# Optimization experiments

Hardware: AMD Instinct MI355X
Metric: run time of the kernel (lower is better)

Reference implementation:

```python
import jax, jax.numpy as jnp
import numpy as np

EPS = 1e-6

def _conv(x, w, padding):
    # x: [B,C,H,W], w: [O,I,kh,kw]
    return jax.lax.conv_general_dilated(x, w, window_strides=(1, 1), padding=padding,
                                        dimension_numbers=('NCHW', 'OIHW', 'NCHW'))

def setup_inputs() -> dict:
    key = jax.random.key(0)
    ks = jax.random.split(key, 8)
    C = 512
    B, H, W = 4, 64, 64
    s1 = 1.0 / np.sqrt(C)          # 1x1 conv fan-in
    s3 = 1.0 / np.sqrt(C * 9)      # 3x3 conv fan-in
    return {
        'x': jax.random.normal(ks[0], (B, C, H, W), dtype=jnp.float32),
        'ln_w': jnp.ones((C,), dtype=jnp.float32),
        'ln_b': jnp.zeros((C,), dtype=jnp.float32),
        'wq': jax.random.normal(ks[1], (C, C, 1, 1), dtype=jnp.float32) * s1,
        'wk': jax.random.normal(ks[2], (C, C, 3, 3), dtype=jnp.float32) * s3,
        'wv': jax.random.normal(ks[3], (C, C, 3, 3), dtype=jnp.float32) * s3,
        'wp': jax.random.normal(ks[4], (C, C, 1, 1), dtype=jnp.float32) * s1,
        'bp': jnp.zeros((C,), dtype=jnp.float32),
    }

def reference(x, ln_w, ln_b, wq, wk, wv, wp, bp):
    # channels_first LayerNorm over C
    u = jnp.mean(x, axis=1, keepdims=True)
    s = jnp.mean((x - u) ** 2, axis=1, keepdims=True)
    h = (x - u) / jnp.sqrt(s + EPS)
    h = ln_w[None, :, None, None] * h + ln_b[None, :, None, None]

    q = _conv(h, wq, 'VALID')           # 1x1
    k = _conv(h, wk, [(1, 1), (1, 1)])  # 3x3, pad 1
    v = _conv(h, wv, [(1, 1), (1, 1)])

    b, c, H, W = q.shape
    hw = H * W
    q = q.reshape(b, c, hw)
    k = k.reshape(b, c, hw)
    v = v.reshape(b, c, hw)

    scale = jnp.asarray(int(c) ** (-0.5), q.dtype)
    attn = jnp.einsum('bcm,bcn->bmn', q, k) * scale  # [b, hw_q, hw_k]
    attn = jax.nn.softmax(attn, axis=2)
    out = jnp.einsum('bcn,bmn->bcm', v, attn)        # [b, c, hw_q]
    out = out.reshape(b, c, H, W)

    out = _conv(out, wp, 'VALID') + bp[None, :, None, None]
    return x + out
```

## Files before the change

kernel.cpp:

```cpp
#include <hip/hip_runtime.h>
#include <hip/hip_bf16.h>

#define C_DIM 512
#define HW    4096
#define BATCH 4
#define PW    66
#define PPIX  (PW*PW)

typedef __attribute__((ext_vector_type(8))) short bf16x8;
typedef __attribute__((ext_vector_type(4))) float f32x4;
typedef __attribute__((ext_vector_type(16))) float f32x16;
typedef __attribute__((ext_vector_type(2))) long long l64x2;

static __device__ __forceinline__ short f2b(float f) {
    union { float f; unsigned u; } v; v.f = f;
    unsigned r = v.u + 0x7fffu + ((v.u >> 16) & 1u);
    return (short)(r >> 16);
}
static __device__ __forceinline__ float b2f(short s) {
    union { unsigned u; float f; } v; v.u = ((unsigned)(unsigned short)s) << 16;
    return v.f;
}

static __device__ __forceinline__ f32x4 zero4() {
    f32x4 v = {0.f, 0.f, 0.f, 0.f};
    return v;
}
static __device__ __forceinline__ f32x16 zero16() {
    f32x16 v = {0.f,0.f,0.f,0.f, 0.f,0.f,0.f,0.f, 0.f,0.f,0.f,0.f, 0.f,0.f,0.f,0.f};
    return v;
}

static __device__ __forceinline__ void gload16(const void* g, void* l) {
    __builtin_amdgcn_global_load_lds(
        (__attribute__((address_space(1))) void*)g,
        (__attribute__((address_space(3))) void*)l, 16, 0, 0);
}

__global__ void k_cvt_bf16(const float* __restrict__ in, short* __restrict__ out, int n) {
    int i = blockIdx.x * 256 + threadIdx.x;
    if (i < n) out[i] = f2b(in[i]);
}

__global__ void k_reorder_w38(const float* __restrict__ w, unsigned char* __restrict__ out) {
    int i = blockIdx.x * 256 + threadIdx.x;
    int o = i / 576;
    int p8 = (i - o * 576) * 8;
    int kc2 = p8 >> 6;
    int tap = kc2 >> 3;
    int p = p8 & 63;
    int g = (p >> 4) & 3, half = (p >> 3) & 1;
    int c0 = (kc2 & 7) * 64 + half * 32 + g * 8;
    const float* src = w + ((size_t)o * 512 + c0) * 9 + tap;
    float f0 = src[0] * 64.f, f1 = src[9] * 64.f, f2 = src[18] * 64.f, f3 = src[27] * 64.f;
    float f4 = src[36] * 64.f, f5 = src[45] * 64.f, f6 = src[54] * 64.f, f7 = src[63] * 64.f;
    int lo = __builtin_amdgcn_cvt_pk_fp8_f32(f0, f1, 0, false);
    lo     = __builtin_amdgcn_cvt_pk_fp8_f32(f2, f3, lo, true);
    int hi = __builtin_amdgcn_cvt_pk_fp8_f32(f4, f5, 0, false);
    hi     = __builtin_amdgcn_cvt_pk_fp8_f32(f6, f7, hi, true);
    *(uint2*)&out[(size_t)o * 4608 + p8] = make_uint2((unsigned)lo, (unsigned)hi);
}

__global__ void k_cvt_h8(const short* __restrict__ hp, unsigned char* __restrict__ out) {
    int i = blockIdx.x * 256 + threadIdx.x;
    int row = i >> 6;
    int p8 = (i & 63) * 8;
    int grp = p8 >> 6;
    int p = p8 & 63;
    int g = (p >> 4) & 3, half = (p >> 3) & 1;
    int c = grp * 64 + half * 32 + g * 8;
    bf16x8 v = *(const bf16x8*)&hp[(size_t)row * 512 + c];
    int lo = __builtin_amdgcn_cvt_pk_fp8_f32(b2f(v[0]), b2f(v[1]), 0, false);
    lo     = __builtin_amdgcn_cvt_pk_fp8_f32(b2f(v[2]), b2f(v[3]), lo, true);
    int hi = __builtin_amdgcn_cvt_pk_fp8_f32(b2f(v[4]), b2f(v[5]), 0, false);
    hi     = __builtin_amdgcn_cvt_pk_fp8_f32(b2f(v[6]), b2f(v[7]), hi, true);
    *(uint2*)&out[(size_t)row * 512 + p8] = make_uint2((unsigned)lo, (unsigned)hi);
}

__global__ void k_cvt_k8(const short* __restrict__ in, unsigned char* __restrict__ out) {
    int i = blockIdx.x * 256 + threadIdx.x;
    int m = i >> 6;
    int p = (i & 63) * 8;
    int kcp = p >> 6, g = (p >> 4) & 3, half = (p >> 3) & 1;
    int chb = (kcp * 2 + half) * 32 + g * 8;
    bf16x8 v = *(const bf16x8*)&in[(size_t)m * 512 + chb];
    int lo = __builtin_amdgcn_cvt_pk_fp8_f32(b2f(v[0]), b2f(v[1]), 0, false);
    lo     = __builtin_amdgcn_cvt_pk_fp8_f32(b2f(v[2]), b2f(v[3]), lo, true);
    int hi = __builtin_amdgcn_cvt_pk_fp8_f32(b2f(v[4]), b2f(v[5]), 0, false);
    hi     = __builtin_amdgcn_cvt_pk_fp8_f32(b2f(v[6]), b2f(v[7]), hi, true);
    *(uint2*)&out[(size_t)m * 512 + p] = make_uint2((unsigned)lo, (unsigned)hi);
}

__global__ void k_ln_fused(const float* __restrict__ x, const float* __restrict__ lnw,
                           const float* __restrict__ lnb, short* __restrict__ hp) {
    __shared__ float red[8][64];
    __shared__ float mean_s[64], rstd_s[64];
    __shared__ short tile[64][65];
    int bid = blockIdx.x;
    int y = bid & 63, b = bid >> 6;
    int t = threadIdx.x;
    int px = t & 63, cg = t >> 6;
    const float* xb = x + (size_t)b * C_DIM * HW + (size_t)y * 64;

    float s = 0.f, sq = 0.f;
    for (int c = cg * 128; c < cg * 128 + 128; ++c) {
        float v = xb[(size_t)c * HW + px];
        s += v; sq += v * v;
    }
    red[cg][px] = s;
    red[4 + cg][px] = sq;
    __syncthreads();
    if (t < 64) {
        float S = red[0][t] + red[1][t] + red[2][t] + red[3][t];
        float Q = red[4][t] + red[5][t] + red[6][t] + red[7][t];
        float mu  = S * (1.0f / C_DIM);
        float var = Q * (1.0f / C_DIM) - mu * mu;
        mean_s[t] = mu;
        rstd_s[t] = 1.0f / sqrtf(var + 1e-6f);
    }
    __syncthreads();
    float mu = mean_s[px], rs = rstd_s[px];
    int cj = t & 63, pj = t >> 6;
    for (int ct = 0; ct < 8; ++ct) {
        int c0 = ct * 64;
        #pragma unroll
        for (int cc = 0; cc < 64; cc += 4) {
            int c = c0 + cc + cg;
            float v = xb[(size_t)c * HW + px];
            tile[cc + cg][px] = f2b((v - mu) * rs * lnw[c] + lnb[c]);
        }
        __syncthreads();
        #pragma unroll
        for (int pp = 0; pp < 64; pp += 4) {
            int pidx = pp + pj;
            size_t dst = ((size_t)b * PPIX + (size_t)(y + 1) * PW + 1 + pidx) * C_DIM + c0 + cj;
            hp[dst] = tile[cj][pidx];
        }
        __syncthreads();
    }
}

template<int TAPS, int GMODE, int EPI>
__global__ __launch_bounds__(256, 2) void k_gemm(
        const short* __restrict__ A, const short* __restrict__ Bw,
        void* __restrict__ Out, const float* __restrict__ bias,
        const float* __restrict__ resid)
{
    constexpr int K = TAPS * 512;
    constexpr int NKC = K / 64;
    __shared__ short Alds[128 * 64];
    __shared__ short Blds[128 * 64];
    int bid = blockIdx.x;
    int mt = bid & 31, nt = (bid >> 5) & 3, b = bid >> 7;
    int m0 = mt * 128, n0 = nt * 128;
    int t = threadIdx.x;
    int lane = t & 63, w = t >> 6;
    int wm = w >> 1, wn = w & 1;
    int g = lane >> 4, li = lane & 15;
    int srow = t >> 3, schunk = t & 7;
    const short* Ab = A + (GMODE == 0 ? (size_t)b * PPIX * C_DIM : (size_t)b * HW * C_DIM);

    f32x4 acc[4][4];
    #pragma unroll
    for (int i = 0; i < 4; ++i)
        #pragma unroll
        for (int j = 0; j < 4; ++j) acc[i][j] = zero4();

    for (int kc = 0; kc < NKC; ++kc) {
        int tap = (TAPS == 9) ? (kc >> 3) : 4;
        int cb  = (kc & 7) * 64;
        __syncthreads();
        #pragma unroll
        for (int r = 0; r < 4; ++r) {
            int row = r * 32 + srow;
            size_t goff;
            if (GMODE == 0) {
                int m = m0 + row;
                int yy = m >> 6, xx = m & 63;
                int pp = (yy + tap / 3) * PW + xx + (tap % 3);
                goff = (size_t)pp * C_DIM + cb + schunk * 8;
            } else {
                goff = (size_t)(m0 + row) * K + kc * 64 + schunk * 8;
            }
            gload16(Ab + goff, Alds + row * 64 + schunk * 8);
        }
        #pragma unroll
        for (int r = 0; r < 4; ++r) {
            int row = r * 32 + srow;
            size_t goff = (size_t)(n0 + row) * K + kc * 64 + schunk * 8;
            gload16(Bw + goff, Blds + row * 64 + schunk * 8);
        }
        __syncthreads();
        #pragma unroll
        for (int ks = 0; ks < 2; ++ks) {
            int koff = ks * 32 + g * 8;
            bf16x8 af[4], bfr[4];
            #pragma unroll
            for (int i = 0; i < 4; ++i)
                af[i] = *(const bf16x8*)&Alds[(wm * 64 + i * 16 + li) * 64 + koff];
            #pragma unroll
            for (int j = 0; j < 4; ++j)
                bfr[j] = *(const bf16x8*)&Blds[(wn * 64 + j * 16 + li) * 64 + koff];
            #pragma unroll
            for (int i = 0; i < 4; ++i)
                #pragma unroll
                for (int j = 0; j < 4; ++j)
                    acc[i][j] = __builtin_amdgcn_mfma_f32_16x16x32_bf16(af[i], bfr[j], acc[i][j], 0, 0, 0);
        }
    }
    #pragma unroll
    for (int fm = 0; fm < 4; ++fm) {
        #pragma unroll
        for (int fn = 0; fn < 4; ++fn) {
            int mrow = m0 + wm * 64 + fm * 16 + g * 4;
            int ncol = n0 + wn * 64 + fn * 16 + li;
            if constexpr (EPI == 0) {
                #pragma unroll
                for (int i = 0; i < 4; ++i) {
                    size_t dst = ((size_t)b * HW + mrow + i) * C_DIM + ncol;
                    ((short*)Out)[dst] = f2b(acc[fm][fn][i]);
                }
            } else if constexpr (EPI == 1) {
                size_t dst = ((size_t)b * C_DIM + ncol) * HW + mrow;
                short4 sv = make_short4(f2b(acc[fm][fn][0]), f2b(acc[fm][fn][1]),
                                        f2b(acc[fm][fn][2]), f2b(acc[fm][fn][3]));
                *(short4*)((short*)Out + dst) = sv;
            } else {
                size_t dst = ((size_t)b * C_DIM + ncol) * HW + mrow;
                float bb = bias[ncol];
                float4 xr = *(const float4*)(resid + dst);
                float4 o;
                o.x = acc[fm][fn][0] + bb + xr.x;
                o.y = acc[fm][fn][1] + bb + xr.y;
                o.z = acc[fm][fn][2] + bb + xr.z;
                o.w = acc[fm][fn][3] + bb + xr.w;
                *(float4*)((float*)Out + dst) = o;
            }
        }
    }
}

__global__ __launch_bounds__(256, 2) void k_gemm_kv8(
        const unsigned char* __restrict__ A8, const unsigned char* __restrict__ Bk8,
        const unsigned char* __restrict__ Bv8, short* __restrict__ OutK,
        short* __restrict__ OutV)
{
    __shared__ unsigned char Alds[2][10240];
    __shared__ unsigned char Bklds[2][10240];
    __shared__ unsigned char Bvlds[2][10240];
    int bid = blockIdx.x;
    int mt = bid & 31, nt = (bid >> 5) & 3, b = bid >> 7;
    int m0 = mt * 128, n0 = nt * 128;
    int t = threadIdx.x;
    int lane = t & 63, w = t >> 6;
    int wm = w >> 1, wn = w & 1;
    int g = lane >> 4, li = lane & 15;
    const unsigned char* Ab = A8 + (size_t)b * PPIX * 512;

    int srowv[3], schv[3];
    #pragma unroll
    for (int r = 0; r < 3; ++r) {
        int slot = r * 256 + t;
        int row = slot / 5;
        int ch = slot - row * 5;
        srowv[r] = row;
        schv[r] = (ch < 4) ? ch * 16 : 0;
    }
    bool act2 = (w < 2);

    f32x4 accK[4][4], accV[4][4];
    #pragma unroll
    for (int i = 0; i < 4; ++i)
        #pragma unroll
        for (int j = 0; j < 4; ++j) { accK[i][j] = zero4(); accV[i][j] = zero4(); }

    auto STAGE = [&](int bf, int kc2) {
        int tap = kc2 >> 3;
        int gofs = (kc2 & 7) * 64;
        int ty3 = tap / 3, tx3 = tap % 3;
        #pragma unroll
        for (int r = 0; r < 3; ++r) {
            if (r < 2 || act2) {
                int row = srowv[r];
                int m = m0 + row;
                int yy = m >> 6, xx = m & 63;
                int pp = (yy + ty3) * PW + xx + tx3;
                int dst = (r * 256 + t) * 16;
                gload16(Ab + (size_t)pp * 512 + gofs + schv[r], &Alds[bf][dst]);
                size_t gb = (size_t)(n0 + row) * 4608 + kc2 * 64 + schv[r];
                gload16(Bk8 + gb, &Bklds[bf][dst]);
                gload16(Bv8 + gb, &Bvlds[bf][dst]);
            }
        }
    };

    auto COMPUTE = [&](int bf) {
        l64x2 av[4], bk[4], bv[4];
        #pragma unroll
        for (int i = 0; i < 4; ++i)
            av[i] = *(const l64x2*)&Alds[bf][(wm * 64 + i * 16 + li) * 80 + g * 16];
        #pragma unroll
        for (int j = 0; j < 4; ++j)
            bk[j] = *(const l64x2*)&Bklds[bf][(wn * 64 + j * 16 + li) * 80 + g * 16];
        #pragma unroll
        for (int j = 0; j < 4; ++j)
            bv[j] = *(const l64x2*)&Bvlds[bf][(wn * 64 + j * 16 + li) * 80 + g * 16];
        #pragma unroll
        for (int h = 0; h < 2; ++h) {
            #pragma unroll
            for (int i = 0; i < 4; ++i)
                #pragma unroll
                for (int j = 0; j < 4; ++j)
                    accK[i][j] = __builtin_amdgcn_mfma_f32_16x16x32_fp8_fp8(
                        av[i][h], bk[j][h], accK[i][j], 0, 0, 0);
            #pragma unroll
            for (int i = 0; i < 4; ++i)
                #pragma unroll
                for (int j = 0; j < 4; ++j)
                    accV[i][j] = __builtin_amdgcn_mfma_f32_16x16x32_fp8_fp8(
                        av[i][h], bv[j][h], accV[i][j], 0, 0, 0);
        }
    };

    STAGE(0, 0);
    __syncthreads();
    int bf = 0;
    for (int kc2 = 0; kc2 < 72; ++kc2) {
        if (kc2 + 1 < 72) STAGE(bf ^ 1, kc2 + 1);
        COMPUTE(bf);
        __syncthreads();
        bf ^= 1;
    }

    const float SCL = 0.015625f;
    #pragma unroll
    for (int fm = 0; fm < 4; ++fm) {
        #pragma unroll
        for (int fn = 0; fn < 4; ++fn) {
            int mrow = m0 + wm * 64 + fm * 16 + g * 4;
            int ncol = n0 + wn * 64 + fn * 16 + li;
            #pragma unroll
            for (int i = 0; i < 4; ++i) {
                size_t dst = ((size_t)b * HW + mrow + i) * C_DIM + ncol;
                OutK[dst] = f2b(accK[fm][fn][i] * SCL);
            }
            size_t dstv = ((size_t)b * C_DIM + ncol) * HW + mrow;
            short4 sv = make_short4(f2b(accV[fm][fn][0] * SCL), f2b(accV[fm][fn][1] * SCL),
                                    f2b(accV[fm][fn][2] * SCL), f2b(accV[fm][fn][3] * SCL));
            *(short4*)(OutV + dstv) = sv;
        }
    }
}

#define KT 32
#define NTILES 64
__global__ __launch_bounds__(512, 2) void k_attn(
        const short* __restrict__ qT, const unsigned char* __restrict__ kT8,
        const short* __restrict__ vg, short* __restrict__ O0,
        short* __restrict__ O1, float* __restrict__ L0, float* __restrict__ L1)
{
    __shared__ __align__(16) short pool[73728];
    unsigned char* Kp8 = (unsigned char*)pool;
    short* Vp = pool + 16384;
    short* Pp = pool + 57344;

    int bid0 = blockIdx.x;
    int bid = (bid0 & 7) * 32 + (bid0 >> 3);
    int qt = bid & 31, ks = (bid >> 5) & 1, b = bid >> 6;
    int m0 = qt * 128;
    int t = threadIdx.x, lane = t & 63, w = t >> 6;
    int g = lane >> 4, li = lane & 15;
    int l31 = lane & 31, l5 = lane >> 5;

    const unsigned char* kb8 = kT8 + ((size_t)b * HW + (size_t)ks * 2048) * 512;
    const short* vb = vg + (size_t)b * C_DIM * HW + ks * 2048;

    long long qf8[16];
    {
        const short* qrow = qT + ((size_t)b * HW + m0 + w * 16 + li) * C_DIM;
        #pragma unroll
        for (int kc = 0; kc < 16; ++kc) {
            bf16x8 qv = *(const bf16x8*)&qrow[kc * 32 + g * 8];
            int lo = __builtin_amdgcn_cvt_pk_fp8_f32(b2f(qv[0]), b2f(qv[1]), 0, false);
            lo     = __builtin_amdgcn_cvt_pk_fp8_f32(b2f(qv[2]), b2f(qv[3]), lo, true);
            int hi = __builtin_amdgcn_cvt_pk_fp8_f32(b2f(qv[4]), b2f(qv[5]), 0, false);
            hi     = __builtin_amdgcn_cvt_pk_fp8_f32(b2f(qv[6]), b2f(qv[7]), hi, true);
            qf8[kc] = ((long long)(unsigned)hi << 32) | (unsigned)lo;
        }
    }
    f32x16 oacc[8];
    #pragma unroll
    for (int a = 0; a < 8; ++a) oacc[a] = zero16();
    float lsum = 0.f;

    const unsigned char* ksrc8 = kb8 + (size_t)(t & 31) * 512 + (t >> 5) * 16;
    int voff[5];
    #pragma unroll
    for (int r = 0; r < 5; ++r) {
        int D = r * 512 + t;
        int ch = D / 5;
        int c  = D - ch * 5;
        voff[r] = (c < 4) ? ch * 4096 + c * 8 : 0;
    }

    const float SC = 0.044194173824159216f * 1.4426950408889634f;

    auto STAGE = [&](int buf, int nt) {
        int n0 = nt * KT;
        const unsigned char* kS = ksrc8 + (size_t)n0 * 512;
        unsigned char* kD = Kp8 + buf * 16384 + t * 16;
        gload16(kS, kD);
        gload16(kS + 256, kD + 8192);
        short* vD = Vp + buf * 20480 + t * 8;
        #pragma unroll
        for (int r = 0; r < 5; ++r)
            gload16(vb + voff[r] + n0, vD + r * 4096);
    };

    STAGE(0, 0);
    asm volatile("s_waitcnt vmcnt(0)" ::: "memory");
    __builtin_amdgcn_s_barrier();
    __builtin_amdgcn_sched_barrier(0);

    int buf = 0;
    for (int nt = 0; nt < NTILES; ++nt) {
        if (nt + 1 < NTILES) STAGE(buf ^ 1, nt + 1);

        const unsigned char* kbase8 = Kp8 + buf * 16384 + g * 512 + li * 16;
        f32x4 s0[2], s1[2];
        s0[0] = zero4(); s0[1] = zero4(); s1[0] = zero4(); s1[1] = zero4();
        __builtin_amdgcn_s_setprio(1);
        #pragma unroll
        for (int kcp = 0; kcp < 8; ++kcp) {
            #pragma unroll
            for (int fn = 0; fn < 2; ++fn) {
                l64x2 kv = *(const l64x2*)&kbase8[kcp * 2048 + fn * 256];
                s0[fn] = __builtin_amdgcn_mfma_f32_16x16x32_fp8_fp8(kv[0], qf8[2 * kcp],     s0[fn], 0, 0, 0);
                s1[fn] = __builtin_amdgcn_mfma_f32_16x16x32_fp8_fp8(kv[1], qf8[2 * kcp + 1], s1[fn], 0, 0, 0);
            }
        }
        __builtin_amdgcn_s_setprio(0);
        #pragma unroll
        for (int fn = 0; fn < 2; ++fn) {
            float e0 = exp2f((s0[fn][0] + s1[fn][0]) * SC);
            float e1 = exp2f((s0[fn][1] + s1[fn][1]) * SC);
            float e2 = exp2f((s0[fn][2] + s1[fn][2]) * SC);
            float e3 = exp2f((s0[fn][3] + s1[fn][3]) * SC);
            lsum += (e0 + e1) + (e2 + e3);
            union { __hip_bfloat162 h; unsigned u; } p01, p23;
            p01.h = __float22bfloat162_rn(make_float2(e0, e1));
            p23.h = __float22bfloat162_rn(make_float2(e2, e3));
            *(uint2*)&Pp[(w * 16 + li) * 40 + fn * 16 + g * 4] = make_uint2(p01.u, p23.u);
        }

        asm volatile("s_waitcnt lgkmcnt(0)" ::: "memory");
        __builtin_amdgcn_s_barrier();
        __builtin_amdgcn_sched_barrier(0);

        const short* vbase = Vp + buf * 20480 + (size_t)w * 64 * 40;
        bf16x8 vf[2][2];
        #pragma unroll
        for (int cht = 0; cht < 2; ++cht)
            #pragma unroll
            for (int kx = 0; kx < 2; ++kx)
                vf[cht][kx] = *(const bf16x8*)&vbase[(cht * 32 + l31) * 40 + kx * 16 + l5 * 8];
        __builtin_amdgcn_s_setprio(1);
        #pragma unroll
        for (int q2 = 0; q2 < 4; ++q2) {
            #pragma unroll
            for (int kx = 0; kx < 2; ++kx) {
                bf16x8 pf = *(const bf16x8*)&Pp[(q2 * 32 + l31) * 40 + kx * 16 + l5 * 8];
                oacc[q2 * 2 + 0] = __builtin_amdgcn_mfma_f32_32x32x16_bf16(vf[0][kx], pf, oacc[q2 * 2 + 0], 0, 0, 0);
                oacc[q2 * 2 + 1] = __builtin_amdgcn_mfma_f32_32x32x16_bf16(vf[1][kx], pf, oacc[q2 * 2 + 1], 0, 0, 0);
            }
        }
        __builtin_amdgcn_s_setprio(0);

        asm volatile("s_waitcnt vmcnt(0)" ::: "memory");
        __builtin_amdgcn_s_barrier();
        __builtin_amdgcn_sched_barrier(0);
        buf ^= 1;
    }

    lsum += __shfl_xor(lsum, 16);
    lsum += __shfl_xor(lsum, 32);
    float* Lb = (ks ? L1 : L0) + (size_t)b * HW + m0 + w * 16;
    if (lane < 16) Lb[lane] = lsum;

    short* tp = pool + w * 9216;
    #pragma unroll
    for (int a = 0; a < 8; ++a) {
        int q2 = a >> 1, cht = a & 1;
        int q_l = q2 * 32 + l31;
        #pragma unroll
        for (int rq = 0; rq < 4; ++rq) {
            int chb = cht * 32 + rq * 8 + l5 * 4;
            union { __hip_bfloat162 h; unsigned u; } x01, x23;
            x01.h = __float22bfloat162_rn(make_float2(oacc[a][rq * 4 + 0], oacc[a][rq * 4 + 1]));
            x23.h = __float22bfloat162_rn(make_float2(oacc[a][rq * 4 + 2], oacc[a][rq * 4 + 3]));
            *(uint2*)&tp[q_l * 72 + chb] = make_uint2(x01.u, x23.u);
        }
    }
    asm volatile("s_waitcnt lgkmcnt(0)" ::: "memory");
    __builtin_amdgcn_sched_barrier(0);
    short* Ob = (ks ? O1 : O0) + ((size_t)b * HW + m0) * C_DIM + w * 64;
    #pragma unroll
    for (int qg = 0; qg < 16; ++qg) {
        int qr = qg * 8 + (lane >> 3);
        bf16x8 v = *(const bf16x8*)&tp[qr * 72 + (lane & 7) * 8];
        *(bf16x8*)&Ob[(size_t)qr * C_DIM + (lane & 7) * 8] = v;
    }
}

__global__ void k_att_comb(const short* __restrict__ O0, const short* __restrict__ O1,
                           const float* __restrict__ L0, const float* __restrict__ L1,
                           short* __restrict__ oatt) {
    int i = blockIdx.x * 256 + threadIdx.x;
    int row = i >> 6;
    int c0 = (i & 63) * 8;
    float r = 1.0f / (L0[row] + L1[row]);
    size_t base = (size_t)row * C_DIM + c0;
    bf16x8 a = *(const bf16x8*)&O0[base];
    bf16x8 c = *(const bf16x8*)&O1[base];
    bf16x8 o;
    #pragma unroll
    for (int j = 0; j < 8; ++j)
        o[j] = f2b((b2f(a[j]) + b2f(c[j])) * r);
    *(bf16x8*)&oatt[base] = o;
}

extern "C" void kernel_launch(void* const* d_in, const int* in_sizes, int n_in,
                              void* d_out, int out_size, void* d_ws, size_t ws_size,
                              hipStream_t stream) {
    const float* x    = (const float*)d_in[0];
    const float* ln_w = (const float*)d_in[1];
    const float* ln_b = (const float*)d_in[2];
    const float* wq   = (const float*)d_in[3];
    const float* wk   = (const float*)d_in[4];
    const float* wv   = (const float*)d_in[5];
    const float* wp   = (const float*)d_in[6];
    const float* bp   = (const float*)d_in[7];
    float* out = (float*)d_out;

    char* ws = (char*)d_ws;
    size_t off = 0;
    auto alloc = [&](size_t bytes) {
        char* p = ws + off;
        off += (bytes + 255) & ~(size_t)255;
        return p;
    };
    short* hp   = (short*)alloc((size_t)BATCH * PPIX * C_DIM * 2);
    unsigned char* hp8 = (unsigned char*)alloc((size_t)BATCH * PPIX * 512);
    short* wqb  = (short*)alloc((size_t)512 * 512 * 2);
    unsigned char* wk8 = (unsigned char*)alloc((size_t)512 * 4608);
    unsigned char* wv8 = (unsigned char*)alloc((size_t)512 * 4608);
    short* wpb  = (short*)alloc((size_t)512 * 512 * 2);
    short* qT   = (short*)alloc((size_t)BATCH * HW * C_DIM * 2);
    short* kT   = (short*)alloc((size_t)BATCH * HW * C_DIM * 2);
    short* vg   = (short*)alloc((size_t)BATCH * HW * C_DIM * 2);
    short* oatt = (short*)alloc((size_t)BATCH * HW * C_DIM * 2);
    float* mean = (float*)alloc((size_t)BATCH * HW * 4);
    float* rstd = (float*)alloc((size_t)BATCH * HW * 4);

    hipMemsetAsync(hp, 0, (size_t)BATCH * PPIX * C_DIM * 2, stream);
    k_cvt_bf16<<<1024, 256, 0, stream>>>(wq, wqb, 512 * 512);
    k_cvt_bf16<<<1024, 256, 0, stream>>>(wp, wpb, 512 * 512);
    k_reorder_w38<<<1152, 256, 0, stream>>>(wk, wk8);
    k_reorder_w38<<<1152, 256, 0, stream>>>(wv, wv8);
    k_ln_fused<<<256, 256, 0, stream>>>(x, ln_w, ln_b, hp);
    k_cvt_h8<<<4356, 256, 0, stream>>>(hp, hp8);

    k_gemm<1, 0, 0><<<512, 256, 0, stream>>>(hp, wqb, qT, nullptr, nullptr);
    k_gemm_kv8<<<512, 256, 0, stream>>>(hp8, wk8, wv8, kT, vg);

    unsigned char* kT8 = hp8;
    k_cvt_k8<<<4096, 256, 0, stream>>>(kT, kT8);

    short* Op0 = hp;
    short* Op1 = oatt;
    float* Ls0 = mean;
    float* Ls1 = rstd;
    k_attn<<<256, 512, 0, stream>>>(qT, kT8, vg, Op0, Op1, Ls0, Ls1);
    k_att_comb<<<4096, 256, 0, stream>>>(Op0, Op1, Ls0, Ls1, oatt);

    k_gemm<1, 1, 2><<<512, 256, 0, stream>>>(oatt, wpb, out, bp, x);
}
```

Measured before the change: 340.4 us.

## Fuse Q projection into FP8 KV conv GEMM and emit FP8 from LayerNorm

LayerNorm now writes the padded FP8 activation buffer directly, which removes the bf16 padded buffer and the separate conversion kernel. The Q 1x1 projection is folded into the K/V 3x3 GEMM in FP8, computed during the center-tap K chunks so it reuses the A tiles already staged there. This removes a separate bf16 Q GEMM launch and its re-read of the activations. It costs more accumulator registers and shared memory in the fused kernel, and Q now carries FP8 precision.

```diff
diff --git a/kernel.cpp b/kernel.cpp
--- a/kernel.cpp
+++ b/kernel.cpp
@@ -61,20 +61,20 @@
     *(uint2*)&out[(size_t)o * 4608 + p8] = make_uint2((unsigned)lo, (unsigned)hi);
 }
 
-__global__ void k_cvt_h8(const short* __restrict__ hp, unsigned char* __restrict__ out) {
+__global__ void k_reorder_w18(const float* __restrict__ w, unsigned char* __restrict__ out) {
     int i = blockIdx.x * 256 + threadIdx.x;
-    int row = i >> 6;
+    int o = i >> 6;
     int p8 = (i & 63) * 8;
     int grp = p8 >> 6;
     int p = p8 & 63;
     int g = (p >> 4) & 3, half = (p >> 3) & 1;
-    int c = grp * 64 + half * 32 + g * 8;
-    bf16x8 v = *(const bf16x8*)&hp[(size_t)row * 512 + c];
-    int lo = __builtin_amdgcn_cvt_pk_fp8_f32(b2f(v[0]), b2f(v[1]), 0, false);
-    lo     = __builtin_amdgcn_cvt_pk_fp8_f32(b2f(v[2]), b2f(v[3]), lo, true);
-    int hi = __builtin_amdgcn_cvt_pk_fp8_f32(b2f(v[4]), b2f(v[5]), 0, false);
-    hi     = __builtin_amdgcn_cvt_pk_fp8_f32(b2f(v[6]), b2f(v[7]), hi, true);
-    *(uint2*)&out[(size_t)row * 512 + p8] = make_uint2((unsigned)lo, (unsigned)hi);
+    int c0 = grp * 64 + half * 32 + g * 8;
+    const float* src = w + (size_t)o * 512 + c0;
+    int lo = __builtin_amdgcn_cvt_pk_fp8_f32(src[0] * 64.f, src[1] * 64.f, 0, false);
+    lo     = __builtin_amdgcn_cvt_pk_fp8_f32(src[2] * 64.f, src[3] * 64.f, lo, true);
+    int hi = __builtin_amdgcn_cvt_pk_fp8_f32(src[4] * 64.f, src[5] * 64.f, 0, false);
+    hi     = __builtin_amdgcn_cvt_pk_fp8_f32(src[6] * 64.f, src[7] * 64.f, hi, true);
+    *(uint2*)&out[(size_t)o * 512 + p8] = make_uint2((unsigned)lo, (unsigned)hi);
 }
 
 __global__ void k_cvt_k8(const short* __restrict__ in, unsigned char* __restrict__ out) {
@@ -92,10 +92,10 @@
 }
 
 __global__ void k_ln_fused(const float* __restrict__ x, const float* __restrict__ lnw,
-                           const float* __restrict__ lnb, short* __restrict__ hp) {
+                           const float* __restrict__ lnb, unsigned char* __restrict__ hp8) {
     __shared__ float red[8][64];
     __shared__ float mean_s[64], rstd_s[64];
-    __shared__ short tile[64][65];
+    __shared__ short tile[64][72];
     int bid = blockIdx.x;
     int y = bid & 63, b = bid >> 6;
     int t = threadIdx.x;
@@ -120,21 +120,27 @@
     }
     __syncthreads();
     float mu = mean_s[px], rs = rstd_s[px];
-    int cj = t & 63, pj = t >> 6;
+    int q8 = t & 7, pxe = t >> 3;
+    int pbyte = (q8 & 3) * 16 + (q8 >> 2) * 8;
     for (int ct = 0; ct < 8; ++ct) {
         int c0 = ct * 64;
         #pragma unroll
         for (int cc = 0; cc < 64; cc += 4) {
             int c = c0 + cc + cg;
             float v = xb[(size_t)c * HW + px];
-            tile[cc + cg][px] = f2b((v - mu) * rs * lnw[c] + lnb[c]);
+            tile[px][cc + cg] = f2b((v - mu) * rs * lnw[c] + lnb[c]);
         }
         __syncthreads();
         #pragma unroll
-        for (int pp = 0; pp < 64; pp += 4) {
-            int pidx = pp + pj;
-            size_t dst = ((size_t)b * PPIX + (size_t)(y + 1) * PW + 1 + pidx) * C_DIM + c0 + cj;
-            hp[dst] = tile[cj][pidx];
+        for (int h = 0; h < 2; ++h) {
+            int pix = pxe + h * 32;
+            bf16x8 v = *(const bf16x8*)&tile[pix][q8 * 8];
+            int lo = __builtin_amdgcn_cvt_pk_fp8_f32(b2f(v[0]), b2f(v[1]), 0, false);
+            lo     = __builtin_amdgcn_cvt_pk_fp8_f32(b2f(v[2]), b2f(v[3]), lo, true);
+            int hi = __builtin_amdgcn_cvt_pk_fp8_f32(b2f(v[4]), b2f(v[5]), 0, false);
+            hi     = __builtin_amdgcn_cvt_pk_fp8_f32(b2f(v[6]), b2f(v[7]), hi, true);
+            size_t row = (size_t)b * PPIX + (size_t)(y + 1) * PW + 1 + pix;
+            *(uint2*)&hp8[row * 512 + c0 + pbyte] = make_uint2((unsigned)lo, (unsigned)hi);
         }
         __syncthreads();
     }
@@ -240,14 +246,15 @@
     }
 }
 
-__global__ __launch_bounds__(256, 2) void k_gemm_kv8(
+__global__ __launch_bounds__(256, 2) void k_gemm_kvq8(
         const unsigned char* __restrict__ A8, const unsigned char* __restrict__ Bk8,
-        const unsigned char* __restrict__ Bv8, short* __restrict__ OutK,
-        short* __restrict__ OutV)
+        const unsigned char* __restrict__ Bv8, const unsigned char* __restrict__ Bq8,
+        short* __restrict__ OutK, short* __restrict__ OutV, short* __restrict__ OutQ)
 {
     __shared__ unsigned char Alds[2][10240];
     __shared__ unsigned char Bklds[2][10240];
     __shared__ unsigned char Bvlds[2][10240];
+    __shared__ unsigned char Bqlds[2][8192];
     int bid = blockIdx.x;
     int mt = bid & 31, nt = (bid >> 5) & 3, b = bid >> 7;
     int m0 = mt * 128, n0 = nt * 128;
@@ -267,12 +274,15 @@
         schv[r] = (ch < 4) ? ch * 16 : 0;
     }
     bool act2 = (w < 2);
-
-    f32x4 accK[4][4], accV[4][4];
+    int qsrow0 = t >> 2, qsch = (t & 3) * 16;
+
+    f32x4 accK[4][4], accV[4][4], accQ[4][4];
     #pragma unroll
     for (int i = 0; i < 4; ++i)
         #pragma unroll
-        for (int j = 0; j < 4; ++j) { accK[i][j] = zero4(); accV[i][j] = zero4(); }
+        for (int j = 0; j < 4; ++j) {
+            accK[i][j] = zero4(); accV[i][j] = zero4(); accQ[i][j] = zero4();
+        }
 
     auto STAGE = [&](int bf, int kc2) {
         int tap = kc2 >> 3;
@@ -292,9 +302,18 @@
                 gload16(Bv8 + gb, &Bvlds[bf][dst]);
             }
         }
+        if (kc2 >= 32 && kc2 < 40) {
+            int gq = (kc2 - 32) * 64;
+            #pragma unroll
+            for (int r = 0; r < 2; ++r) {
+                int row = r * 64 + qsrow0;
+                gload16(Bq8 + (size_t)(n0 + row) * 512 + gq + qsch,
+                        &Bqlds[bf][(r * 256 + t) * 16]);
+            }
+        }
     };
 
-    auto COMPUTE = [&](int bf) {
+    auto COMPUTE = [&](int bf, bool qwin) {
         l64x2 av[4], bk[4], bv[4];
         #pragma unroll
         for (int i = 0; i < 4; ++i)
@@ -320,6 +339,20 @@
                     accV[i][j] = __builtin_amdgcn_mfma_f32_16x16x32_fp8_fp8(
                         av[i][h], bv[j][h], accV[i][j], 0, 0, 0);
         }
+        if (qwin) {
+            l64x2 bq[4];
+            #pragma unroll
+            for (int j = 0; j < 4; ++j)
+                bq[j] = *(const l64x2*)&Bqlds[bf][(wn * 64 + j * 16 + li) * 64 + g * 16];
+            #pragma unroll
+            for (int h = 0; h < 2; ++h)
+                #pragma unroll
+                for (int i = 0; i < 4; ++i)
+                    #pragma unroll
+                    for (int j = 0; j < 4; ++j)
+                        accQ[i][j] = __builtin_amdgcn_mfma_f32_16x16x32_fp8_fp8(
+                            av[i][h], bq[j][h], accQ[i][j], 0, 0, 0);
+        }
     };
 
     STAGE(0, 0);
@@ -327,7 +360,7 @@
     int bf = 0;
     for (int kc2 = 0; kc2 < 72; ++kc2) {
         if (kc2 + 1 < 72) STAGE(bf ^ 1, kc2 + 1);
-        COMPUTE(bf);
+        COMPUTE(bf, kc2 >= 32 && kc2 < 40);
         __syncthreads();
         bf ^= 1;
     }
@@ -343,6 +376,7 @@
             for (int i = 0; i < 4; ++i) {
                 size_t dst = ((size_t)b * HW + mrow + i) * C_DIM + ncol;
                 OutK[dst] = f2b(accK[fm][fn][i] * SCL);
+                OutQ[dst] = f2b(accQ[fm][fn][i] * SCL);
             }
             size_t dstv = ((size_t)b * C_DIM + ncol) * HW + mrow;
             short4 sv = make_short4(f2b(accV[fm][fn][0] * SCL), f2b(accV[fm][fn][1] * SCL),
@@ -549,9 +583,9 @@
         off += (bytes + 255) & ~(size_t)255;
         return p;
     };
-    short* hp   = (short*)alloc((size_t)BATCH * PPIX * C_DIM * 2);
+    short* hp   = (short*)alloc((size_t)BATCH * HW * C_DIM * 2);
     unsigned char* hp8 = (unsigned char*)alloc((size_t)BATCH * PPIX * 512);
-    short* wqb  = (short*)alloc((size_t)512 * 512 * 2);
+    unsigned char* wq8 = (unsigned char*)alloc((size_t)512 * 512);
     unsigned char* wk8 = (unsigned char*)alloc((size_t)512 * 4608);
     unsigned char* wv8 = (unsigned char*)alloc((size_t)512 * 4608);
     short* wpb  = (short*)alloc((size_t)512 * 512 * 2);
@@ -562,16 +596,14 @@
     float* mean = (float*)alloc((size_t)BATCH * HW * 4);
     float* rstd = (float*)alloc((size_t)BATCH * HW * 4);
 
-    hipMemsetAsync(hp, 0, (size_t)BATCH * PPIX * C_DIM * 2, stream);
-    k_cvt_bf16<<<1024, 256, 0, stream>>>(wq, wqb, 512 * 512);
+    hipMemsetAsync(hp8, 0, (size_t)BATCH * PPIX * 512, stream);
     k_cvt_bf16<<<1024, 256, 0, stream>>>(wp, wpb, 512 * 512);
+    k_reorder_w18<<<128, 256, 0, stream>>>(wq, wq8);
     k_reorder_w38<<<1152, 256, 0, stream>>>(wk, wk8);
     k_reorder_w38<<<1152, 256, 0, stream>>>(wv, wv8);
-    k_ln_fused<<<256, 256, 0, stream>>>(x, ln_w, ln_b, hp);
-    k_cvt_h8<<<4356, 256, 0, stream>>>(hp, hp8);
-
-    k_gemm<1, 0, 0><<<512, 256, 0, stream>>>(hp, wqb, qT, nullptr, nullptr);
-    k_gemm_kv8<<<512, 256, 0, stream>>>(hp8, wk8, wv8, kT, vg);
+    k_ln_fused<<<256, 256, 0, stream>>>(x, ln_w, ln_b, hp8);
+
+    k_gemm_kvq8<<<512, 256, 0, stream>>>(hp8, wk8, wv8, wq8, kT, vg, qT);
 
     unsigned char* kT8 = hp8;
     k_cvt_k8<<<4096, 256, 0, stream>>>(kT, kT8);
```

Result: slower. 368.2 us (+8.2%).
